# Performance work log

Hardware: AMD Instinct MI355X
Metric: run time of the kernel (lower is better)

Reference implementation:

```python
import jax, jax.numpy as jnp
import numpy as np

DT = 0.01          # Euler step size
ALPHA = 1.0        # Grubb exponent (hardcoded in forward())
V0 = 0.02          # resting venous blood volume fraction
NOISE_AMP = 0.01   # amplitude of per-step noise injected into the neural drive
T = 1000           # integration length (hardcoded in forward())
B = 16384          # batch of independent simulations


def setup_inputs() -> dict:
    key = jax.random.key(0)
    noise = jax.random.normal(key, (T, B), dtype=jnp.float32)
    f32 = lambda v: jnp.asarray(v, dtype=jnp.float32)
    return {
        "noise": noise,
        "sigma": f32(0.9),
        "mu": f32(0.8),
        "lamb": f32(0.3),
        "beta": f32(0.9),
        "psi": f32(0.5),
        "phi": f32(2.0),
        "chi": f32(0.3),
    }


def reference(noise, sigma, mu, lamb, beta, psi, phi, chi):
    # Balloon-Windkessel BOLD model, explicit Euler, per-step noise.
    # States per simulation: s (vasodilatory signal), f (flow), v (volume), q (dHb).
    b = noise.shape[1]
    inv_alpha = 1.0 / ALPHA

    def step(carry, z):
        s, f, v, q = carry
        # oxygen extraction fraction E(f) = 1 - (1 - E0)^(1/f)
        E = 1.0 - (1.0 - beta) ** (1.0 / f)
        v_a = v ** inv_alpha  # outflow v^(1/alpha)
        s2 = s + DT * (NOISE_AMP * z - sigma * s - mu * (f - 1.0))
        f2 = f + DT * s
        v2 = v + DT * (f - v_a) / lamb
        q2 = q + DT * (f * E / beta - v_a * q / v) / lamb
        # BOLD readout at the new state
        y = V0 * (phi * (1.0 - q2) + psi * (1.0 - q2 / v2) + chi * (1.0 - v2))
        return (s2, f2, v2, q2), y

    init = (
        jnp.zeros((b,), noise.dtype),
        jnp.ones((b,), noise.dtype),
        jnp.ones((b,), noise.dtype),
        jnp.ones((b,), noise.dtype),
    )
    _, ys = jax.lax.scan(step, init, noise)  # ys: [T, B]
    return ys
```

## Files before the change

### kernel.cpp

```cpp
#include <hip/hip_runtime.h>


#define BATCH     16384
#define DT        0.01f
#define NOISE_AMP 0.01f
#define V0        0.02f
#define CHUNKS    40
#define CL        25
#define GSIMS     16
#define NTHREADS  (CHUNKS * GSIMS)
#define LEVELS    6

#if __has_builtin(__builtin_amdgcn_exp2f)
#define EXP2F(x) __builtin_amdgcn_exp2f(x)
#else
#define EXP2F(x) exp2f(x)
#endif

__device__ __forceinline__ float uf(float x) {
    return __uint_as_float(__builtin_amdgcn_readfirstlane(__float_as_uint(x)));
}

struct D22 { double a, b, c, d; };
__device__ __forceinline__ D22 dmul(D22 x, D22 y) {
    D22 r;
    r.a = x.a * y.a + x.b * y.c;  r.b = x.a * y.b + x.b * y.d;
    r.c = x.c * y.a + x.d * y.c;  r.d = x.c * y.b + x.d * y.d;
    return r;
}

__global__ __launch_bounds__(NTHREADS, 6) void balloon_scan(
    const float* __restrict__ noise,
    const float* __restrict__ p_sigma,
    const float* __restrict__ p_mu,
    const float* __restrict__ p_lamb,
    const float* __restrict__ p_beta,
    const float* __restrict__ p_psi,
    const float* __restrict__ p_phi,
    const float* __restrict__ p_chi,
    float* __restrict__ out)
{
    const int tid = threadIdx.x;
    const int g   = tid & (GSIMS - 1);
    const int cc  = tid >> 4;
    const int sim = blockIdx.x * GSIMS + g;

    const float sigma = uf(p_sigma[0]);
    const float mu    = uf(p_mu[0]);
    const float lamb  = uf(p_lamb[0]);
    const float beta  = uf(p_beta[0]);
    const float psi   = uf(p_psi[0]);
    const float phi   = uf(p_phi[0]);
    const float chi   = uf(p_chi[0]);

    const float as_   = 1.0f - DT * sigma;
    const float dtn   = DT * NOISE_AMP;
    const float dtm   = DT * mu;
    const float dt_il = uf((float)(0.01 / (double)lamb));
    const float av    = 1.0f - dt_il;
    const float kq    = uf(dt_il / beta);
    const float lc    = uf(log2f(1.0f - beta));
    const float c0 = V0 * (phi + psi + chi), c1 = V0 * phi, c2 = V0 * psi, c3 = V0 * chi;

    D22 A; A.a = 1.0 - 0.01 * (double)sigma; A.b = -0.01 * (double)mu;
           A.c = 0.01;                       A.d = 1.0;
    D22 A2 = dmul(A, A), A4 = dmul(A2, A2), A8 = dmul(A4, A4);
    D22 A16 = dmul(A8, A8);
    D22 P = dmul(dmul(A16, A8), A);
    double avd = 1.0 - 0.01 / (double)lamb;
    double av2 = avd * avd, av4 = av2 * av2, av8 = av4 * av4;
    double av16 = av8 * av8;
    double ap = av16 * av8 * avd;

    float M11[LEVELS], M12[LEVELS], M21[LEVELS], M22[LEVELS], AVP[LEVELS];
#pragma unroll
    for (int j = 0; j < LEVELS; ++j) {
        M11[j] = uf((float)P.a); M12[j] = uf((float)P.b);
        M21[j] = uf((float)P.c); M22[j] = uf((float)P.d);
        AVP[j] = uf((float)ap);
        P = dmul(P, P); ap = ap * ap;
    }

    float ws = 0.0f, wf = 1.0f, avc = 1.0f;
#pragma unroll
    for (int j = 0; j < LEVELS; ++j) {
        if ((cc >> j) & 1) {
            float t = __builtin_fmaf(M11[j], ws, M12[j] * wf);
            wf = __builtin_fmaf(M21[j], ws, M22[j] * wf);
            ws = t;
            avc *= AVP[j];
        }
    }

    __shared__ float sA[NTHREADS];
    __shared__ float sB[NTHREADS];

    const float* zp = noise + cc * (CL * BATCH) + sim;

    float zr[CL];
#pragma unroll
    for (int j = 0; j < CL; ++j)
        zr[j] = __builtin_nontemporal_load(&zp[j * BATCH]);

    float rs = 0.0f, rf = 0.0f;
#pragma unroll
    for (int j = 0; j < CL; ++j) {
        const float u = __builtin_fmaf(dtn, zr[j], dtm);
        const float t = __builtin_fmaf(as_, rs, __builtin_fmaf(-dtm, rf, u));
        rf = __builtin_fmaf(DT, rs, rf);
        rs = t;
    }

    sA[tid] = rs; sB[tid] = rf;
    __syncthreads();
#pragma unroll
    for (int j = 0; j < LEVELS; ++j) {
        const int off = 1 << j;
        float ns = 0.0f, nf = 0.0f;
        const bool has = (cc >= off);
        if (has) { ns = sA[tid - off * GSIMS]; nf = sB[tid - off * GSIMS]; }
        __syncthreads();
        if (has) {
            rs = __builtin_fmaf(M11[j], ns, __builtin_fmaf(M12[j], nf, rs));
            rf = __builtin_fmaf(M21[j], ns, __builtin_fmaf(M22[j], nf, rf));
            sA[tid] = rs; sB[tid] = rf;
        }
        __syncthreads();
    }
    float s0 = ws, f0 = wf;
    if (cc > 0) { s0 += sA[tid - GSIMS]; f0 += sB[tid - GSIMS]; }
    __syncthreads();

    float s = s0, f = f0, Rv = 0.0f, Rq = 0.0f;
#pragma unroll
    for (int j = 0; j < CL; ++j) {
        const float zf   = zr[j];
        const float invf = __builtin_amdgcn_rcpf(f);
        const float e2   = EXP2F(lc * invf);
        const float t1   = __builtin_fmaf(-f, e2, f);
        Rv = __builtin_fmaf(av, Rv, dt_il * f);
        Rq = __builtin_fmaf(av, Rq, kq * t1);
        zr[j] = f;
        const float s2 = __builtin_fmaf(as_, s,
                         __builtin_fmaf(dtn, zf,
                         __builtin_fmaf(-dtm, f, dtm)));
        f = __builtin_fmaf(DT, s, f);
        s = s2;
    }

    sA[tid] = Rv; sB[tid] = Rq;
    __syncthreads();
#pragma unroll
    for (int j = 0; j < LEVELS; ++j) {
        const int off = 1 << j;
        float nv = 0.0f, nq = 0.0f;
        const bool has = (cc >= off);
        if (has) { nv = sA[tid - off * GSIMS]; nq = sB[tid - off * GSIMS]; }
        __syncthreads();
        if (has) {
            Rv = __builtin_fmaf(AVP[j], nv, Rv);
            Rq = __builtin_fmaf(AVP[j], nq, Rq);
            sA[tid] = Rv; sB[tid] = Rq;
        }
        __syncthreads();
    }
    float v = avc, q = avc;
    if (cc > 0) { v += sA[tid - GSIMS]; q += sB[tid - GSIMS]; }

    float* op = out + cc * (CL * BATCH) + sim;
#pragma unroll
    for (int j = 0; j < CL; ++j) {
        const float fj   = zr[j];
        const float invf = __builtin_amdgcn_rcpf(fj);
        const float e2   = EXP2F(lc * invf);
        const float t1   = __builtin_fmaf(-fj, e2, fj);
        const float vn   = __builtin_fmaf(av, v, dt_il * fj);
        const float qn   = __builtin_fmaf(av, q, kq * t1);
        const float invv = __builtin_amdgcn_rcpf(vn);
        const float y = __builtin_fmaf(-c2, qn * invv,
                        __builtin_fmaf(-c3, vn,
                        __builtin_fmaf(-c1, qn, c0)));
        __builtin_nontemporal_store(y, &op[j * BATCH]);
        v = vn; q = qn;
    }
}

extern "C" void kernel_launch(void* const* d_in, const int* in_sizes, int n_in,
                              void* d_out, int out_size, void* d_ws, size_t ws_size,
                              hipStream_t stream) {
    const float* noise   = (const float*)d_in[0];
    const float* p_sigma = (const float*)d_in[1];
    const float* p_mu    = (const float*)d_in[2];
    const float* p_lamb  = (const float*)d_in[3];
    const float* p_beta  = (const float*)d_in[4];
    const float* p_psi   = (const float*)d_in[5];
    const float* p_phi   = (const float*)d_in[6];
    const float* p_chi   = (const float*)d_in[7];

    balloon_scan<<<BATCH / GSIMS, NTHREADS, 0, stream>>>(
        noise, p_sigma, p_mu, p_lamb, p_beta, p_psi, p_phi, p_chi,
        (float*)d_out);
}
```

Before: 163.9 us.

## Process two simulations per thread and re-read noise instead of caching in registers

Each thread now handles two adjacent simulations using float2 vector loads, stores and shared-memory scans, which halves the block count and the scan overhead per simulation. The per-thread register cache of the noise chunk is removed. Noise is re-read from global memory in each of the three passes, and the flow trajectory is recomputed in the final pass instead of being stored. This trades register pressure for extra global reads and recomputation, and lowers the occupancy hint from 6 to 5.

```diff
diff --git a/kernel.cpp b/kernel.cpp
--- a/kernel.cpp
+++ b/kernel.cpp
@@ -7,9 +7,12 @@
 #define V0        0.02f
 #define CHUNKS    40
 #define CL        25
-#define GSIMS     16
-#define NTHREADS  (CHUNKS * GSIMS)
+#define LANES     16
+#define GSIMS     (LANES * 2)
+#define NTHREADS  (CHUNKS * LANES)
 #define LEVELS    6
+
+typedef float f2 __attribute__((ext_vector_type(2)));
 
 #if __has_builtin(__builtin_amdgcn_exp2f)
 #define EXP2F(x) __builtin_amdgcn_exp2f(x)
@@ -29,7 +32,7 @@
     return r;
 }
 
-__global__ __launch_bounds__(NTHREADS, 6) void balloon_scan(
+__global__ __launch_bounds__(NTHREADS, 5) void balloon_scan(
     const float* __restrict__ noise,
     const float* __restrict__ p_sigma,
     const float* __restrict__ p_mu,
@@ -41,9 +44,9 @@
     float* __restrict__ out)
 {
     const int tid = threadIdx.x;
-    const int g   = tid & (GSIMS - 1);
+    const int g   = tid & (LANES - 1);
     const int cc  = tid >> 4;
-    const int sim = blockIdx.x * GSIMS + g;
+    const int sim = blockIdx.x * GSIMS + 2 * g;
 
     const float sigma = uf(p_sigma[0]);
     const float mu    = uf(p_mu[0]);
@@ -92,96 +95,152 @@
         }
     }
 
-    __shared__ float sA[NTHREADS];
-    __shared__ float sB[NTHREADS];
+    __shared__ f2 sA[NTHREADS];
+    __shared__ f2 sB[NTHREADS];
 
     const float* zp = noise + cc * (CL * BATCH) + sim;
 
-    float zr[CL];
-#pragma unroll
-    for (int j = 0; j < CL; ++j)
-        zr[j] = __builtin_nontemporal_load(&zp[j * BATCH]);
-
-    float rs = 0.0f, rf = 0.0f;
-#pragma unroll
+    float rs0 = 0.0f, rf0 = 0.0f, rs1 = 0.0f, rf1 = 0.0f;
+#pragma unroll 5
     for (int j = 0; j < CL; ++j) {
-        const float u = __builtin_fmaf(dtn, zr[j], dtm);
-        const float t = __builtin_fmaf(as_, rs, __builtin_fmaf(-dtm, rf, u));
-        rf = __builtin_fmaf(DT, rs, rf);
-        rs = t;
-    }
-
-    sA[tid] = rs; sB[tid] = rf;
+        const f2 z = *reinterpret_cast<const f2*>(zp + j * BATCH);
+        {
+            const float u = __builtin_fmaf(dtn, z.x, dtm);
+            const float t = __builtin_fmaf(as_, rs0, __builtin_fmaf(-dtm, rf0, u));
+            rf0 = __builtin_fmaf(DT, rs0, rf0);
+            rs0 = t;
+        }
+        {
+            const float u = __builtin_fmaf(dtn, z.y, dtm);
+            const float t = __builtin_fmaf(as_, rs1, __builtin_fmaf(-dtm, rf1, u));
+            rf1 = __builtin_fmaf(DT, rs1, rf1);
+            rs1 = t;
+        }
+    }
+
+    sA[tid] = (f2){rs0, rs1}; sB[tid] = (f2){rf0, rf1};
     __syncthreads();
 #pragma unroll
     for (int j = 0; j < LEVELS; ++j) {
         const int off = 1 << j;
-        float ns = 0.0f, nf = 0.0f;
+        f2 ns = (f2){0.0f, 0.0f}, nf = (f2){0.0f, 0.0f};
         const bool has = (cc >= off);
-        if (has) { ns = sA[tid - off * GSIMS]; nf = sB[tid - off * GSIMS]; }
+        if (has) { ns = sA[tid - off * LANES]; nf = sB[tid - off * LANES]; }
         __syncthreads();
         if (has) {
-            rs = __builtin_fmaf(M11[j], ns, __builtin_fmaf(M12[j], nf, rs));
-            rf = __builtin_fmaf(M21[j], ns, __builtin_fmaf(M22[j], nf, rf));
-            sA[tid] = rs; sB[tid] = rf;
-        }
-        __syncthreads();
-    }
-    float s0 = ws, f0 = wf;
-    if (cc > 0) { s0 += sA[tid - GSIMS]; f0 += sB[tid - GSIMS]; }
+            rs0 = __builtin_fmaf(M11[j], ns.x, __builtin_fmaf(M12[j], nf.x, rs0));
+            rf0 = __builtin_fmaf(M21[j], ns.x, __builtin_fmaf(M22[j], nf.x, rf0));
+            rs1 = __builtin_fmaf(M11[j], ns.y, __builtin_fmaf(M12[j], nf.y, rs1));
+            rf1 = __builtin_fmaf(M21[j], ns.y, __builtin_fmaf(M22[j], nf.y, rf1));
+            sA[tid] = (f2){rs0, rs1}; sB[tid] = (f2){rf0, rf1};
+        }
+        __syncthreads();
+    }
+    float s00 = ws, f00 = wf, s01 = ws, f01 = wf;
+    if (cc > 0) {
+        const f2 pa = sA[tid - LANES], pb = sB[tid - LANES];
+        s00 += pa.x; f00 += pb.x;
+        s01 += pa.y; f01 += pb.y;
+    }
     __syncthreads();
 
-    float s = s0, f = f0, Rv = 0.0f, Rq = 0.0f;
-#pragma unroll
+    float s0 = s00, f0 = f00, s1 = s01, f1 = f01;
+    float Rv0 = 0.0f, Rq0 = 0.0f, Rv1 = 0.0f, Rq1 = 0.0f;
+#pragma unroll 5
     for (int j = 0; j < CL; ++j) {
-        const float zf   = zr[j];
-        const float invf = __builtin_amdgcn_rcpf(f);
-        const float e2   = EXP2F(lc * invf);
-        const float t1   = __builtin_fmaf(-f, e2, f);
-        Rv = __builtin_fmaf(av, Rv, dt_il * f);
-        Rq = __builtin_fmaf(av, Rq, kq * t1);
-        zr[j] = f;
-        const float s2 = __builtin_fmaf(as_, s,
-                         __builtin_fmaf(dtn, zf,
-                         __builtin_fmaf(-dtm, f, dtm)));
-        f = __builtin_fmaf(DT, s, f);
-        s = s2;
-    }
-
-    sA[tid] = Rv; sB[tid] = Rq;
+        const f2 z = *reinterpret_cast<const f2*>(zp + j * BATCH);
+        {
+            const float invf = __builtin_amdgcn_rcpf(f0);
+            const float e2   = EXP2F(lc * invf);
+            const float t1   = __builtin_fmaf(-f0, e2, f0);
+            Rv0 = __builtin_fmaf(av, Rv0, dt_il * f0);
+            Rq0 = __builtin_fmaf(av, Rq0, kq * t1);
+            const float s2 = __builtin_fmaf(as_, s0,
+                             __builtin_fmaf(dtn, z.x,
+                             __builtin_fmaf(-dtm, f0, dtm)));
+            f0 = __builtin_fmaf(DT, s0, f0);
+            s0 = s2;
+        }
+        {
+            const float invf = __builtin_amdgcn_rcpf(f1);
+            const float e2   = EXP2F(lc * invf);
+            const float t1   = __builtin_fmaf(-f1, e2, f1);
+            Rv1 = __builtin_fmaf(av, Rv1, dt_il * f1);
+            Rq1 = __builtin_fmaf(av, Rq1, kq * t1);
+            const float s2 = __builtin_fmaf(as_, s1,
+                             __builtin_fmaf(dtn, z.y,
+                             __builtin_fmaf(-dtm, f1, dtm)));
+            f1 = __builtin_fmaf(DT, s1, f1);
+            s1 = s2;
+        }
+    }
+
+    sA[tid] = (f2){Rv0, Rv1}; sB[tid] = (f2){Rq0, Rq1};
     __syncthreads();
 #pragma unroll
     for (int j = 0; j < LEVELS; ++j) {
         const int off = 1 << j;
-        float nv = 0.0f, nq = 0.0f;
+        f2 nv = (f2){0.0f, 0.0f}, nq = (f2){0.0f, 0.0f};
         const bool has = (cc >= off);
-        if (has) { nv = sA[tid - off * GSIMS]; nq = sB[tid - off * GSIMS]; }
+        if (has) { nv = sA[tid - off * LANES]; nq = sB[tid - off * LANES]; }
         __syncthreads();
         if (has) {
-            Rv = __builtin_fmaf(AVP[j], nv, Rv);
-            Rq = __builtin_fmaf(AVP[j], nq, Rq);
-            sA[tid] = Rv; sB[tid] = Rq;
-        }
-        __syncthreads();
-    }
-    float v = avc, q = avc;
-    if (cc > 0) { v += sA[tid - GSIMS]; q += sB[tid - GSIMS]; }
-
+            Rv0 = __builtin_fmaf(AVP[j], nv.x, Rv0);
+            Rq0 = __builtin_fmaf(AVP[j], nq.x, Rq0);
+            Rv1 = __builtin_fmaf(AVP[j], nv.y, Rv1);
+            Rq1 = __builtin_fmaf(AVP[j], nq.y, Rq1);
+            sA[tid] = (f2){Rv0, Rv1}; sB[tid] = (f2){Rq0, Rq1};
+        }
+        __syncthreads();
+    }
+    float v0 = avc, q0 = avc, v1 = avc, q1 = avc;
+    if (cc > 0) {
+        const f2 pv = sA[tid - LANES], pq = sB[tid - LANES];
+        v0 += pv.x; q0 += pq.x;
+        v1 += pv.y; q1 += pq.y;
+    }
+
+    s0 = s00; f0 = f00; s1 = s01; f1 = f01;
     float* op = out + cc * (CL * BATCH) + sim;
-#pragma unroll
+#pragma unroll 5
     for (int j = 0; j < CL; ++j) {
-        const float fj   = zr[j];
-        const float invf = __builtin_amdgcn_rcpf(fj);
-        const float e2   = EXP2F(lc * invf);
-        const float t1   = __builtin_fmaf(-fj, e2, fj);
-        const float vn   = __builtin_fmaf(av, v, dt_il * fj);
-        const float qn   = __builtin_fmaf(av, q, kq * t1);
-        const float invv = __builtin_amdgcn_rcpf(vn);
-        const float y = __builtin_fmaf(-c2, qn * invv,
-                        __builtin_fmaf(-c3, vn,
-                        __builtin_fmaf(-c1, qn, c0)));
-        __builtin_nontemporal_store(y, &op[j * BATCH]);
-        v = vn; q = qn;
+        const f2 z = *reinterpret_cast<const f2*>(zp + j * BATCH);
+        f2 y;
+        {
+            const float invf = __builtin_amdgcn_rcpf(f0);
+            const float e2   = EXP2F(lc * invf);
+            const float t1   = __builtin_fmaf(-f0, e2, f0);
+            const float vn   = __builtin_fmaf(av, v0, dt_il * f0);
+            const float qn   = __builtin_fmaf(av, q0, kq * t1);
+            const float s2 = __builtin_fmaf(as_, s0,
+                             __builtin_fmaf(dtn, z.x,
+                             __builtin_fmaf(-dtm, f0, dtm)));
+            f0 = __builtin_fmaf(DT, s0, f0);
+            s0 = s2;
+            const float invv = __builtin_amdgcn_rcpf(vn);
+            y.x = __builtin_fmaf(-c2, qn * invv,
+                  __builtin_fmaf(-c3, vn,
+                  __builtin_fmaf(-c1, qn, c0)));
+            v0 = vn; q0 = qn;
+        }
+        {
+            const float invf = __builtin_amdgcn_rcpf(f1);
+            const float e2   = EXP2F(lc * invf);
+            const float t1   = __builtin_fmaf(-f1, e2, f1);
+            const float vn   = __builtin_fmaf(av, v1, dt_il * f1);
+            const float qn   = __builtin_fmaf(av, q1, kq * t1);
+            const float s2 = __builtin_fmaf(as_, s1,
+                             __builtin_fmaf(dtn, z.y,
+                             __builtin_fmaf(-dtm, f1, dtm)));
+            f1 = __builtin_fmaf(DT, s1, f1);
+            s1 = s2;
+            const float invv = __builtin_amdgcn_rcpf(vn);
+            y.y = __builtin_fmaf(-c2, qn * invv,
+                  __builtin_fmaf(-c3, vn,
+                  __builtin_fmaf(-c1, qn, c0)));
+            v1 = vn; q1 = qn;
+        }
+        __builtin_nontemporal_store(y, reinterpret_cast<f2*>(op + j * BATCH));
     }
 }
 
```

Result: faster. 141.3 us (-13.8%).

## Stage noise tile into LDS via async global_load_lds instead of registers

Applied to the files above, without the earlier changes.

The noise tile for each block (1000 steps x 16 sims, 64KB) is now copied straight into shared memory with global_load_lds direct-to-LDS loads, issued before the parameter setup so the copy overlaps that work. The per-thread 25-element register array is replaced by LDS reads, and the same LDS slots are reused to hold the flow values between passes. This is meant to cut register pressure and improve load coalescing (16-byte loads). In exchange it uses 64KB of LDS per block, which limits occupancy, adds LDS traffic, lowers the occupancy hint to 5 and only partially unrolls the loops.

```diff
diff --git a/kernel.cpp b/kernel.cpp
--- a/kernel.cpp
+++ b/kernel.cpp
@@ -7,15 +7,21 @@
 #define V0        0.02f
 #define CHUNKS    40
 #define CL        25
+#define LANES     16
 #define GSIMS     16
-#define NTHREADS  (CHUNKS * GSIMS)
+#define NTHREADS  (CHUNKS * LANES)
 #define LEVELS    6
+#define ZROWS     1000
+#define ZTILE     (ZROWS * GSIMS)
 
 #if __has_builtin(__builtin_amdgcn_exp2f)
 #define EXP2F(x) __builtin_amdgcn_exp2f(x)
 #else
 #define EXP2F(x) exp2f(x)
 #endif
+
+#define AS1(p) ((__attribute__((address_space(1))) void*)(p))
+#define AS3(p) ((__attribute__((address_space(3))) void*)(p))
 
 __device__ __forceinline__ float uf(float x) {
     return __uint_as_float(__builtin_amdgcn_readfirstlane(__float_as_uint(x)));
@@ -29,7 +35,7 @@
     return r;
 }
 
-__global__ __launch_bounds__(NTHREADS, 6) void balloon_scan(
+__global__ __launch_bounds__(NTHREADS, 5) void balloon_scan(
     const float* __restrict__ noise,
     const float* __restrict__ p_sigma,
     const float* __restrict__ p_mu,
@@ -41,9 +47,31 @@
     float* __restrict__ out)
 {
     const int tid = threadIdx.x;
-    const int g   = tid & (GSIMS - 1);
+    const int g   = tid & (LANES - 1);
     const int cc  = tid >> 4;
-    const int sim = blockIdx.x * GSIMS + g;
+    const int sim0 = blockIdx.x * GSIMS;
+    const int sim  = sim0 + g;
+
+    __shared__ float zt[ZTILE];
+    __shared__ float sA[NTHREADS];
+    __shared__ float sB[NTHREADS];
+
+    {
+        const int wid  = tid >> 6;
+        const int lane = tid & 63;
+        for (int i = wid; i < 62; i += 10) {
+            const int t = 16 * i + (lane >> 2);
+            const int s = (lane & 3) * 4;
+            const float* gp = noise + (size_t)t * BATCH + sim0 + s;
+            __builtin_amdgcn_global_load_lds(AS1(gp), AS3(&zt[i * 256]), 16, 0, 0);
+        }
+        if (wid < 2) {
+            const int t = 992 + 4 * wid + (lane >> 4);
+            const int s = lane & 15;
+            const float* gp = noise + (size_t)t * BATCH + sim0 + s;
+            __builtin_amdgcn_global_load_lds(AS1(gp), AS3(&zt[15872 + wid * 64]), 4, 0, 0);
+        }
+    }
 
     const float sigma = uf(p_sigma[0]);
     const float mu    = uf(p_mu[0]);
@@ -92,20 +120,15 @@
         }
     }
 
-    __shared__ float sA[NTHREADS];
-    __shared__ float sB[NTHREADS];
-
-    const float* zp = noise + cc * (CL * BATCH) + sim;
-
-    float zr[CL];
-#pragma unroll
-    for (int j = 0; j < CL; ++j)
-        zr[j] = __builtin_nontemporal_load(&zp[j * BATCH]);
+    __syncthreads();
+
+    const int zbase = (cc * CL) * GSIMS + g;
 
     float rs = 0.0f, rf = 0.0f;
-#pragma unroll
+#pragma unroll 5
     for (int j = 0; j < CL; ++j) {
-        const float u = __builtin_fmaf(dtn, zr[j], dtm);
+        const float z = zt[zbase + j * GSIMS];
+        const float u = __builtin_fmaf(dtn, z, dtm);
         const float t = __builtin_fmaf(as_, rs, __builtin_fmaf(-dtm, rf, u));
         rf = __builtin_fmaf(DT, rs, rf);
         rs = t;
@@ -118,7 +141,7 @@
         const int off = 1 << j;
         float ns = 0.0f, nf = 0.0f;
         const bool has = (cc >= off);
-        if (has) { ns = sA[tid - off * GSIMS]; nf = sB[tid - off * GSIMS]; }
+        if (has) { ns = sA[tid - off * LANES]; nf = sB[tid - off * LANES]; }
         __syncthreads();
         if (has) {
             rs = __builtin_fmaf(M11[j], ns, __builtin_fmaf(M12[j], nf, rs));
@@ -128,21 +151,22 @@
         __syncthreads();
     }
     float s0 = ws, f0 = wf;
-    if (cc > 0) { s0 += sA[tid - GSIMS]; f0 += sB[tid - GSIMS]; }
+    if (cc > 0) { s0 += sA[tid - LANES]; f0 += sB[tid - LANES]; }
     __syncthreads();
 
     float s = s0, f = f0, Rv = 0.0f, Rq = 0.0f;
-#pragma unroll
+#pragma unroll 5
     for (int j = 0; j < CL; ++j) {
-        const float zf   = zr[j];
+        const int idx = zbase + j * GSIMS;
+        const float z = zt[idx];
         const float invf = __builtin_amdgcn_rcpf(f);
         const float e2   = EXP2F(lc * invf);
         const float t1   = __builtin_fmaf(-f, e2, f);
         Rv = __builtin_fmaf(av, Rv, dt_il * f);
         Rq = __builtin_fmaf(av, Rq, kq * t1);
-        zr[j] = f;
+        zt[idx] = f;
         const float s2 = __builtin_fmaf(as_, s,
-                         __builtin_fmaf(dtn, zf,
+                         __builtin_fmaf(dtn, z,
                          __builtin_fmaf(-dtm, f, dtm)));
         f = __builtin_fmaf(DT, s, f);
         s = s2;
@@ -155,7 +179,7 @@
         const int off = 1 << j;
         float nv = 0.0f, nq = 0.0f;
         const bool has = (cc >= off);
-        if (has) { nv = sA[tid - off * GSIMS]; nq = sB[tid - off * GSIMS]; }
+        if (has) { nv = sA[tid - off * LANES]; nq = sB[tid - off * LANES]; }
         __syncthreads();
         if (has) {
             Rv = __builtin_fmaf(AVP[j], nv, Rv);
@@ -165,12 +189,12 @@
         __syncthreads();
     }
     float v = avc, q = avc;
-    if (cc > 0) { v += sA[tid - GSIMS]; q += sB[tid - GSIMS]; }
+    if (cc > 0) { v += sA[tid - LANES]; q += sB[tid - LANES]; }
 
     float* op = out + cc * (CL * BATCH) + sim;
-#pragma unroll
+#pragma unroll 5
     for (int j = 0; j < CL; ++j) {
-        const float fj   = zr[j];
+        const float fj   = zt[zbase + j * GSIMS];
         const float invf = __builtin_amdgcn_rcpf(fj);
         const float e2   = EXP2F(lc * invf);
         const float t1   = __builtin_fmaf(-fj, e2, fj);
@@ -180,7 +204,7 @@
         const float y = __builtin_fmaf(-c2, qn * invv,
                         __builtin_fmaf(-c3, vn,
                         __builtin_fmaf(-c1, qn, c0)));
-        __builtin_nontemporal_store(y, &op[j * BATCH]);
+        __builtin_nontemporal_store(y, op + j * BATCH);
         v = vn; q = qn;
     }
 }
```

New measurement: 149.0 us. 1.1x faster.
